# Performance work log

Measured on AMD Instinct MI355X. Metric: run time of the kernel, lower is better.

## Reference

```python
import jax, jax.numpy as jnp
import numpy as np

INPUT_DIM = 64
OUTPUT_DIM = 128
KNN = 10          # hardcoded min(10, N) in source
RADIUS = 0.02     # density radius in source


def setup_inputs() -> dict:
    key = jax.random.key(0)
    k1, k2, k3, k4, k5, k6, k7 = jax.random.split(key, 7)
    B, N = 2, 8192
    points = jax.random.uniform(k1, (B, N, 3), dtype=jnp.float32)
    features = jax.random.normal(k2, (B, N, INPUT_DIM), dtype=jnp.float32)
    leaf_mask = jax.random.randint(k3, (B, N), 0, 2) > 0
    d_in = INPUT_DIM + 6
    s1 = 1.0 / np.sqrt(d_in)
    s2 = 1.0 / np.sqrt(OUTPUT_DIM)
    W1 = jax.random.uniform(k4, (d_in, OUTPUT_DIM), jnp.float32, -s1, s1)
    b1 = jax.random.uniform(k5, (OUTPUT_DIM,), jnp.float32, -s1, s1)
    W2 = jax.random.uniform(k6, (OUTPUT_DIM, OUTPUT_DIM), jnp.float32, -s2, s2)
    b2 = jax.random.uniform(k7, (OUTPUT_DIM,), jnp.float32, -s2, s2)
    return {"points": points, "features": features, "leaf_mask": leaf_mask,
            "W1": W1, "b1": b1, "W2": W2, "b2": b2}


def _leaf_geometry(points, mask):
    # points: [N,3], mask: [N] bool -> [N,6]
    mask_f = mask.astype(points.dtype)
    cnt = jnp.maximum(mask_f.sum(), 1.0)
    center = (points * mask_f[:, None]).sum(0) / cnt      # mean of masked points
    rel = points - center                                  # [N,3]
    dist_c = jnp.linalg.norm(rel, axis=1)                  # dist to leaf center
    rel_h = rel[:, 2]                                      # relative height
    horiz = jnp.linalg.norm(rel[:, :2], axis=1)            # horizontal distance
    # pairwise euclidean distances [N,N]; used only for thresholding and knn
    sq = jnp.sum(points * points, axis=1)
    d2 = sq[:, None] + sq[None, :] - 2.0 * (points @ points.T)
    dist = jax.lax.stop_gradient(jnp.sqrt(jnp.maximum(d2, 0.0)))
    density = jnp.sum((dist < RADIUS) & mask[None, :], axis=1).astype(points.dtype)
    # KNN (smallest distances, includes self) -> local PCA curvature
    _, idx = jax.lax.top_k(-dist, KNN)                     # [N,KNN]
    neighbors = points[idx]                                # [N,KNN,3]
    centered = neighbors - points[:, None, :]
    cov = jnp.einsum('nki,nkj->nij', centered, centered) / float(KNN)  # [N,3,3]
    ev = jnp.linalg.eigh(cov)[0]                           # ascending eigenvalues
    curv = ev[:, 0] / (ev[:, 2] + 1e-8)
    rad = jnp.arctan2(rel[:, 1], rel[:, 0])
    geom = jnp.stack([dist_c, rel_h, horiz, density, curv, rad], axis=1)
    # source returns zeros when mask is empty
    return jnp.where(mask_f.sum() > 0, geom, jnp.zeros_like(geom))


def reference(points, features, leaf_mask, W1, b1, W2, b2):
    geom = jax.vmap(_leaf_geometry)(points, leaf_mask)     # [B,N,6]
    combined = jnp.concatenate([features, geom], axis=-1)  # [B,N,input_dim+6]
    h = jax.nn.relu(combined @ W1 + b1)
    return jax.nn.relu(h @ W2 + b2)                        # [B,N,output_dim]
```

## Files before the change

kernel.cpp:

```cpp
#include <hip/hip_runtime.h>
#include <math.h>
#include <stdint.h>

#define B_SZ   2
#define N_PTS  8192
#define IN_DIM 64
#define D_IN   70
#define ODIM   128
#define NQ_ALL (B_SZ * N_PTS)
#define RADIUS_F 0.02f

#define GDIM  32
#define NCELL (GDIM * GDIM * GDIM)
#define HCELL 0.03125f

#define SUP     4
#define NSUP_AX 8
#define NSUPER  (NSUP_AX * NSUP_AX * NSUP_AX)
#define SCAP    352
#define LCAP    24
#define MAXROWS 100

#define MROWS   32

typedef unsigned long long u64;

__device__ __forceinline__ void insert11(u64 (&best)[11], u64 key) {
#pragma unroll
  for (int j = 10; j >= 1; --j) {
    u64 hi = (best[j - 1] > key) ? best[j - 1] : key;
    best[j] = (best[j] < hi) ? best[j] : hi;
  }
  best[0] = (best[0] < key) ? best[0] : key;
}
__device__ __forceinline__ void insert10(u64 (&best)[10], u64 key) {
#pragma unroll
  for (int j = 9; j >= 1; --j) {
    u64 hi = (best[j - 1] > key) ? best[j - 1] : key;
    best[j] = (best[j] < hi) ? best[j] : hi;
  }
  best[0] = (best[0] < key) ? best[0] : key;
}

__device__ __forceinline__ float sq3(float x, float y, float z) {
  return __fadd_rn(__fadd_rn(__fmul_rn(x, x), __fmul_rn(y, y)), __fmul_rn(z, z));
}

__device__ __forceinline__ int cellOf(float v) {
  int c = (int)(v * 32.0f);
  return min(max(c, 0), GDIM - 1);
}

__device__ __forceinline__ void geom_epilogue(const float* __restrict__ P,
                                              const int (&idxs)[10], float dens,
                                              float px, float py, float pz,
                                              float4 ctr, float* __restrict__ g) {
  double c00 = 0, c01 = 0, c02 = 0, c11 = 0, c12 = 0, c22 = 0;
#pragma unroll
  for (int j = 0; j < 10; ++j) {
    const int idx = idxs[j];
    const float nx = P[3 * idx + 0], ny = P[3 * idx + 1], nz = P[3 * idx + 2];
    const float ex = __fsub_rn(nx, px);
    const float ey = __fsub_rn(ny, py);
    const float ez = __fsub_rn(nz, pz);
    c00 += (double)ex * ex; c01 += (double)ex * ey; c02 += (double)ex * ez;
    c11 += (double)ey * ey; c12 += (double)ey * ez; c22 += (double)ez * ez;
  }
  const double a00 = c00 / 10.0, a01 = c01 / 10.0, a02 = c02 / 10.0;
  const double a11 = c11 / 10.0, a12 = c12 / 10.0, a22 = c22 / 10.0;

  double p1 = a01 * a01 + a02 * a02 + a12 * a12;
  double qq = (a00 + a11 + a22) / 3.0;
  double p2 = (a00 - qq) * (a00 - qq) + (a11 - qq) * (a11 - qq) +
              (a22 - qq) * (a22 - qq) + 2.0 * p1;
  double ev0, ev2;
  if (p2 <= 1e-60) {
    ev0 = ev2 = qq;
  } else {
    double p = sqrt(p2 / 6.0);
    double invp = 1.0 / p;
    double b00 = (a00 - qq) * invp, b11 = (a11 - qq) * invp, b22 = (a22 - qq) * invp;
    double b01 = a01 * invp, b02 = a02 * invp, b12 = a12 * invp;
    double detB = b00 * (b11 * b22 - b12 * b12) - b01 * (b01 * b22 - b12 * b02) +
                  b02 * (b01 * b12 - b11 * b02);
    double r = 0.5 * detB;
    r = fmin(1.0, fmax(-1.0, r));
    double phi = acos(r) / 3.0;
    ev2 = qq + 2.0 * p * cos(phi);
    ev0 = qq + 2.0 * p * cos(phi + 2.0943951023931953);
  }
  const float curv = (float)(ev0 / (ev2 + 1e-08));

  const bool on = ctr.w > 0.0f;
  const float rx = __fsub_rn(px, ctr.x);
  const float ry = __fsub_rn(py, ctr.y);
  const float rz = __fsub_rn(pz, ctr.z);
  const float dist_c = sqrtf(sq3(rx, ry, rz));
  const float horiz  = sqrtf(__fadd_rn(__fmul_rn(rx, rx), __fmul_rn(ry, ry)));
  const float rad    = atan2f(ry, rx);

  g[0] = on ? dist_c : 0.0f;
  g[1] = on ? rz : 0.0f;
  g[2] = on ? horiz : 0.0f;
  g[3] = on ? dens : 0.0f;
  g[4] = on ? curv : 0.0f;
  g[5] = on ? rad : 0.0f;
}

__global__ __launch_bounds__(256) void k_build(const float* __restrict__ points,
                                               const int* __restrict__ mask,
                                               int* __restrict__ count,
                                               double* __restrict__ ctrAcc) {
  const int t = blockIdx.x * 256 + threadIdx.x;
  const int b = t >> 13;
  const int i = t & (N_PTS - 1);
  const float* P = points + (size_t)b * N_PTS * 3;
  const float x = P[3 * i + 0], y = P[3 * i + 1], z = P[3 * i + 2];
  atomicAdd(&count[b * NCELL + (cellOf(z) * GDIM + cellOf(y)) * GDIM + cellOf(x)], 1);

  const bool m = mask[b * N_PTS + i] != 0;
  double vx = m ? (double)x : 0.0, vy = m ? (double)y : 0.0;
  double vz = m ? (double)z : 0.0, vc = m ? 1.0 : 0.0;
#pragma unroll
  for (int s = 1; s < 64; s <<= 1) {
    vx += __shfl_xor(vx, s); vy += __shfl_xor(vy, s);
    vz += __shfl_xor(vz, s); vc += __shfl_xor(vc, s);
  }
  __shared__ double sh[4][4];
  const int w = threadIdx.x >> 6;
  if ((threadIdx.x & 63) == 0) { sh[0][w] = vx; sh[1][w] = vy; sh[2][w] = vz; sh[3][w] = vc; }
  __syncthreads();
  if (threadIdx.x == 0) {
    atomicAdd(&ctrAcc[b * 4 + 0], sh[0][0] + sh[0][1] + sh[0][2] + sh[0][3]);
    atomicAdd(&ctrAcc[b * 4 + 1], sh[1][0] + sh[1][1] + sh[1][2] + sh[1][3]);
    atomicAdd(&ctrAcc[b * 4 + 2], sh[2][0] + sh[2][1] + sh[2][2] + sh[2][3]);
    atomicAdd(&ctrAcc[b * 4 + 3], sh[3][0] + sh[3][1] + sh[3][2] + sh[3][3]);
  }
}

__global__ __launch_bounds__(1024) void k_scan(const int* __restrict__ count,
                                               int* __restrict__ start,
                                               int* __restrict__ cur,
                                               const double* __restrict__ ctrAcc,
                                               float* __restrict__ centerOut) {
  const int b = blockIdx.x;
  const int t = threadIdx.x;
  if (t == 0) {
    const float cf = (float)ctrAcc[b * 4 + 3];
    const float div = fmaxf(cf, 1.0f);
    centerOut[b * 4 + 0] = (float)ctrAcc[b * 4 + 0] / div;
    centerOut[b * 4 + 1] = (float)ctrAcc[b * 4 + 1] / div;
    centerOut[b * 4 + 2] = (float)ctrAcc[b * 4 + 2] / div;
    centerOut[b * 4 + 3] = (cf > 0.0f) ? 1.0f : 0.0f;
  }
  int c[32]; int sum = 0;
#pragma unroll
  for (int j = 0; j < 32; ++j) { c[j] = count[b * NCELL + t * 32 + j]; sum += c[j]; }
  __shared__ int s[1024];
  s[t] = sum;
  __syncthreads();
  for (int off = 1; off < 1024; off <<= 1) {
    int v = (t >= off) ? s[t - off] : 0;
    __syncthreads();
    if (t >= off) s[t] += v;
    __syncthreads();
  }
  int excl = (t > 0) ? s[t - 1] : 0;
#pragma unroll
  for (int j = 0; j < 32; ++j) {
    start[b * (NCELL + 1) + t * 32 + j] = excl;
    cur[b * NCELL + t * 32 + j] = excl;
    excl += c[j];
  }
  if (t == 1023) start[b * (NCELL + 1) + NCELL] = excl;
}

__global__ __launch_bounds__(256) void k_scatter(const float* __restrict__ points,
                                                 const int* __restrict__ mask,
                                                 int* __restrict__ cur,
                                                 float4* __restrict__ sorted) {
  const int t = blockIdx.x * 256 + threadIdx.x;
  const int b = t >> 13;
  const int i = t & (N_PTS - 1);
  const float* P = points + (size_t)b * N_PTS * 3;
  const float x = P[3 * i + 0], y = P[3 * i + 1], z = P[3 * i + 2];
  const int cell = (cellOf(z) * GDIM + cellOf(y)) * GDIM + cellOf(x);
  const int pos = atomicAdd(&cur[b * NCELL + cell], 1);
  const unsigned wb = (unsigned)i | ((mask[b * N_PTS + i] != 0) ? 0x80000000u : 0u);
  sorted[(size_t)b * N_PTS + pos] = make_float4(x, y, z, __uint_as_float(wb));
}

__global__ __launch_bounds__(128) void k_collect(const float* __restrict__ points,
                                                 const float4* __restrict__ sorted,
                                                 const int* __restrict__ start,
                                                 const float* __restrict__ center,
                                                 float* __restrict__ geom,
                                                 int* __restrict__ list,
                                                 int* __restrict__ listCnt,
                                                 float COLLECT_T, float DENS_T,
                                                 float THR_CHECK) {
  const int b  = blockIdx.y;
  const int sc = blockIdx.x;
  const int sx = sc & 7, sy = (sc >> 3) & 7, sz = sc >> 6;
  const int tid = threadIdx.x;

  const int* ST = start + b * (NCELL + 1);
  const float4* SP = sorted + (size_t)b * N_PTS;

  const int x0 = SUP * sx, x1 = SUP * sx + SUP - 1;
  const int y0 = SUP * sy, y1 = SUP * sy + SUP - 1;
  const int z0 = SUP * sz, z1 = SUP * sz + SUP - 1;
  const int hx0 = max(x0 - 3, 0), hx1 = min(x1 + 3, GDIM - 1);
  const int hy0 = max(y0 - 3, 0), hy1 = min(y1 + 3, GDIM - 1);
  const int hz0 = max(z0 - 3, 0), hz1 = min(z1 + 3, GDIM - 1);
  const int yc = hy1 - hy0 + 1;
  const int R  = (hz1 - hz0 + 1) * yc;

  __shared__ int    rs[MAXROWS], rp[MAXROWS + 1];
  __shared__ int    qs_[16], qp_[17];
  __shared__ float4 pts4[SCAP];
  __shared__ u64    lbuf[128 * LCAP];

  if (tid < 64) {
    {
      int qlen = 0, qst = 0;
      if (tid < 16) {
        const int z = z0 + (tid >> 2), y = y0 + (tid & 3);
        const int base = (z * GDIM + y) * GDIM;
        qst  = ST[base + x0];
        qlen = ST[base + x1 + 1] - qst;
      }
      int inc = qlen;
      for (int off = 1; off < 64; off <<= 1) { int v = __shfl_up(inc, off); if (tid >= off) inc += v; }
      if (tid < 16) { qs_[tid] = qst; qp_[tid] = inc - qlen; }
      if (tid == 63) qp_[16] = inc;
    }
    {
      int len[2] = {0, 0}, st2[2] = {0, 0};
#pragma unroll
      for (int k = 0; k < 2; ++k) {
        const int r = tid * 2 + k;
        if (r < R) {
          const int z = hz0 + r / yc, y = hy0 + r % yc;
          const int base = (z * GDIM + y) * GDIM;
          st2[k] = ST[base + hx0];
          len[k] = ST[base + hx1 + 1] - st2[k];
        }
      }
      int sum = len[0] + len[1];
      int inc = sum;
      for (int off = 1; off < 64; off <<= 1) { int v = __shfl_up(inc, off); if (tid >= off) inc += v; }
      int exc = inc - sum;
#pragma unroll
      for (int k = 0; k < 2; ++k) {
        const int r = tid * 2 + k;
        if (r < R) { rs[r] = st2[k]; rp[r] = exc; }
        exc += len[k];
      }
      if (tid == 63) rp[R] = inc;
    }
  }
  __syncthreads();

  const int C    = rp[R];
  const int qtot = qp_[16];
  if (qtot == 0) return;

  if (C > SCAP) {
    for (int t = tid; t < qtot; t += 128) {
      int lo = 0, hi = 15;
      while (lo < hi) { const int mid = (lo + hi + 1) >> 1; if (qp_[mid] <= t) lo = mid; else hi = mid - 1; }
      const int qglob = qs_[lo] + (t - qp_[lo]);
      const int pos = atomicAdd(listCnt, 1);
      list[pos] = (b << 13) | qglob;
    }
    return;
  }

  for (int i = tid; i < C; i += 128) {
    int lo = 0, hi = R - 1;
    while (lo < hi) { const int mid = (lo + hi + 1) >> 1; if (rp[mid] <= i) lo = mid; else hi = mid - 1; }
    pts4[i] = SP[rs[lo] + (i - rp[lo])];
  }
  __syncthreads();

  const float4 ctr = reinterpret_cast<const float4*>(center)[b];
  const float* P = points + (size_t)b * N_PTS * 3;
  const int sub = tid & 3;
  const int gq  = tid >> 2;

  for (int q0 = 0; q0 < qtot; q0 += 32) {
    const int myq = q0 + gq;
    const bool act = (myq < qtot);
    const int mq = act ? myq : 0;
    int lo = 0, hi = 15;
    while (lo < hi) { const int mid = (lo + hi + 1) >> 1; if (qp_[mid] <= mq) lo = mid; else hi = mid - 1; }
    const int qglob = qs_[lo] + (mq - qp_[lo]);
    const float4 qp4 = SP[qglob];
    const int qidx = (int)(__float_as_uint(qp4.w) & 0x7FFFFFFFu);
    const float px = qp4.x, py = qp4.y, pz = qp4.z;
    const float sqq = sq3(px, py, pz);

    int cnt = 0;
    u64* myb = &lbuf[tid * LCAP];
#pragma unroll 2
    for (int j = sub; j < C; j += 4) {
      const float4 tp = pts4[j];
      const float sqc = sq3(tp.x, tp.y, tp.z);
      const float dot = __fmaf_rn(pz, tp.z, __fmaf_rn(py, tp.y, __fmul_rn(px, tp.x)));
      const float d2  = __fsub_rn(__fadd_rn(sqq, sqc), __fmul_rn(2.0f, dot));
      const float d2c = fmaxf(d2, 0.0f);
      if (d2c < COLLECT_T) {
        if (cnt < LCAP) {
          const unsigned wb = __float_as_uint(tp.w);
          myb[cnt] = ((u64)__float_as_uint(d2c) << 32)
                   | (u64)(((wb & 0x7FFFFFFFu) << 1) | (wb >> 31));
        }
        ++cnt;
      }
    }

    u64 best[11];
#pragma unroll
    for (int j = 0; j < 11; ++j) best[j] = ~0ull;
    float dens = 0.0f;
    const int m = min(cnt, LCAP);
    for (int i = 0; i < m; ++i) {
      const u64 e = myb[i];
      if ((e & 1ull) && __uint_as_float((unsigned)(e >> 32)) < DENS_T) dens += 1.0f;
      if (e < best[10]) insert11(best, e);
    }
    int cntg = cnt;
    int over = (cnt > LCAP) ? 1 : 0;
#pragma unroll
    for (int s = 1; s < 4; s <<= 1) {
      dens += __shfl_xor(dens, s);
      cntg += __shfl_xor(cntg, s);
      over |= __shfl_xor(over, s);
      u64 ok[11];
#pragma unroll
      for (int j = 0; j < 11; ++j) ok[j] = __shfl_xor(best[j], s);
#pragma unroll
      for (int j = 0; j < 11; ++j) {
        if (ok[j] < best[10]) insert11(best, ok[j]); else break;
      }
    }

    if (act && sub == 0) {
      const float dist9 = sqrtf(__uint_as_float((unsigned)(best[9] >> 32)));
      bool bad = (over != 0) || (cntg < 10) || !(dist9 < THR_CHECK);
      if (cntg >= 11) {
        const float dist10 = sqrtf(__uint_as_float((unsigned)(best[10] >> 32)));
        bad = bad || (dist10 == dist9);
      }
      if (bad) {
        const int pos = atomicAdd(listCnt, 1);
        list[pos] = (b << 13) | qglob;
      } else {
        int idxs[10];
#pragma unroll
        for (int j = 0; j < 10; ++j) idxs[j] = (int)(((unsigned)best[j]) >> 1);
        geom_epilogue(P, idxs, dens, px, py, pz, ctr,
                      geom + ((size_t)b * N_PTS + qidx) * 6);
      }
    }
  }
}

__global__ __launch_bounds__(64) void k_wavefb(const float* __restrict__ points,
                                               const float4* __restrict__ sorted,
                                               const int* __restrict__ start,
                                               const float* __restrict__ center,
                                               float* __restrict__ geom,
                                               int* __restrict__ flags2,
                                               const int* __restrict__ list,
                                               const int* __restrict__ listCnt) {
  const int lane = threadIdx.x;
  const int n = *listCnt;
  for (int it = blockIdx.x; it < n; it += gridDim.x) {
    const int e = list[it];
    const int b = e >> 13, qs = e & (N_PTS - 1);
    const float4* SP = sorted + (size_t)b * N_PTS;
    const int* ST = start + b * (NCELL + 1);
    const float4 qp = SP[qs];
    const int qidx = (int)(__float_as_uint(qp.w) & 0x7FFFFFFFu);
    const float px = qp.x, py = qp.y, pz = qp.z;
    const float sqq = sq3(px, py, pz);
    const int cx = cellOf(px), cy = cellOf(py), cz = cellOf(pz);
    const int xlo = max(cx - 8, 0), xhi = min(cx + 8, GDIM - 1);
    const int ylo = max(cy - 8, 0), yhi = min(cy + 8, GDIM - 1);
    const int zlo = max(cz - 8, 0), zhi = min(cz + 8, GDIM - 1);
    const int ycw = yhi - ylo + 1;
    const int Rw = (zhi - zlo + 1) * ycw;

    u64 best[10];
#pragma unroll
    for (int j = 0; j < 10; ++j) best[j] = ((u64)0x7F800000u << 32) | 0xFFFFFFFFu;
    float dens = 0.0f;

    for (int r = lane; r < Rw; r += 64) {
      const int z = zlo + r / ycw, y = ylo + r % ycw;
      const int base = (z * GDIM + y) * GDIM;
      const int j0 = ST[base + xlo], j1 = ST[base + xhi + 1];
      for (int j = j0; j < j1; ++j) {
        const float4 tp = SP[j];
        const unsigned wb = __float_as_uint(tp.w);
        const float sqc = sq3(tp.x, tp.y, tp.z);
        const float dot = __fmaf_rn(pz, tp.z, __fmaf_rn(py, tp.y, __fmul_rn(px, tp.x)));
        const float d2  = __fsub_rn(__fadd_rn(sqq, sqc), __fmul_rn(2.0f, dot));
        const float dist = sqrtf(fmaxf(d2, 0.0f));
        if ((dist < RADIUS_F) && (wb & 0x80000000u)) dens += 1.0f;
        const u64 key = ((u64)__float_as_uint(dist) << 32) | (wb & 0x7FFFFFFFu);
        if (key < best[9]) insert10(best, key);
      }
    }
#pragma unroll
    for (int s = 1; s < 64; s <<= 1) {
      dens += __shfl_xor(dens, s);
      u64 ok[10];
#pragma unroll
      for (int j = 0; j < 10; ++j) ok[j] = __shfl_xor(best[j], s);
#pragma unroll
      for (int j = 0; j < 10; ++j) {
        if (ok[j] < best[9]) insert10(best, ok[j]); else break;
      }
    }
    if (lane == 0) {
      const float dist9 = __uint_as_float((unsigned)(best[9] >> 32));
      if (dist9 < 0.2494f) {
        const float4 ctr = reinterpret_cast<const float4*>(center)[b];
        const float* P = points + (size_t)b * N_PTS * 3;
        int idxs[10];
#pragma unroll
        for (int j = 0; j < 10; ++j) idxs[j] = (int)(((unsigned)best[j]) & 0x7FFFFFFFu);
        geom_epilogue(P, idxs, dens, px, py, pz, ctr, geom + ((size_t)b * N_PTS + qidx) * 6);
      } else {
        flags2[b * N_PTS + qs] = 1;
      }
    }
  }
}

__global__ __launch_bounds__(256) void k_fallback(const float* __restrict__ points,
                                                  const float4* __restrict__ sorted,
                                                  const int* __restrict__ start,
                                                  const float* __restrict__ center,
                                                  float* __restrict__ geom,
                                                  const int* __restrict__ flags2) {
  const int b = blockIdx.y;
  const int qs = blockIdx.x * 256 + threadIdx.x;
  if (flags2[b * N_PTS + qs] == 0) return;
  const float4 qp = sorted[(size_t)b * N_PTS + qs];
  const unsigned qw = __float_as_uint(qp.w);
  const int qidx = (int)(qw & 0x7FFFFFFFu);

  const float px = qp.x, py = qp.y, pz = qp.z;
  const float sqq = sq3(px, py, pz);
  const int cx = cellOf(px), cy = cellOf(py), cz = cellOf(pz);

  const int* ST = start + b * (NCELL + 1);
  const float4* SP = sorted + (size_t)b * N_PTS;

  u64 best[10];
#pragma unroll
  for (int j = 0; j < 10; ++j) best[j] = ((u64)0x7F800000u << 32) | 0xFFFFFFFFu;
  float dens = 0.0f;

  for (int rho = 0; rho < GDIM; ++rho) {
    const int zlo = max(cz - rho, 0), zhi = min(cz + rho, GDIM - 1);
    const int ylo = max(cy - rho, 0), yhi = min(cy + rho, GDIM - 1);
    for (int z = zlo; z <= zhi; ++z) {
      const int adz = abs(z - cz);
      for (int y = ylo; y <= yhi; ++y) {
        const int ady = abs(y - cy);
        const int m2 = max(adz, ady);
        int ja, jb;
        int ja2 = 0, jb2 = 0;
        const int rowBase = (z * GDIM + y) * GDIM;
        if (m2 == rho) {
          const int xa = max(cx - rho, 0), xb = min(cx + rho, GDIM - 1);
          ja = ST[rowBase + xa]; jb = ST[rowBase + xb + 1];
        } else {
          ja = jb = 0;
          if (cx - rho >= 0)        { ja = ST[rowBase + cx - rho]; jb = ST[rowBase + cx - rho + 1]; }
          if (cx + rho <= GDIM - 1) { ja2 = ST[rowBase + cx + rho]; jb2 = ST[rowBase + cx + rho + 1]; }
        }
#pragma unroll 1
        for (int pass = 0; pass < 2; ++pass) {
          const int j0 = pass ? ja2 : ja;
          const int j1 = pass ? jb2 : jb;
          for (int j = j0; j < j1; ++j) {
            const float4 tp = SP[j];
            const unsigned wb = __float_as_uint(tp.w);
            const float sqc = sq3(tp.x, tp.y, tp.z);
            const float dot = __fmaf_rn(pz, tp.z, __fmaf_rn(py, tp.y, __fmul_rn(px, tp.x)));
            const float d2  = __fsub_rn(__fadd_rn(sqq, sqc), __fmul_rn(2.0f, dot));
            const float dist = sqrtf(fmaxf(d2, 0.0f));
            if ((dist < RADIUS_F) && (wb & 0x80000000u)) dens += 1.0f;
            const u64 key = ((u64)__float_as_uint(dist) << 32) | (wb & 0x7FFFFFFFu);
            if (key < best[9]) insert10(best, key);
          }
        }
      }
    }
    if (rho >= 1) {
      const float dist9 = __uint_as_float((unsigned)(best[9] >> 32));
      if (dist9 < (float)rho * HCELL * 0.999f) break;
    }
  }

  const float4 ctr = reinterpret_cast<const float4*>(center)[b];
  const float* P = points + (size_t)b * N_PTS * 3;
  int idxs[10];
#pragma unroll
  for (int j = 0; j < 10; ++j) idxs[j] = (int)(((unsigned)best[j]) & 0x7FFFFFFFu);
  geom_epilogue(P, idxs, dens, px, py, pz, ctr, geom + ((size_t)b * N_PTS + qidx) * 6);
}

__global__ __launch_bounds__(256) void k_mlp(const float* __restrict__ features,
                                             const float* __restrict__ geom,
                                             const float* __restrict__ W1,
                                             const float* __restrict__ b1,
                                             const float* __restrict__ W2,
                                             const float* __restrict__ b2,
                                             float* __restrict__ out) {
  __shared__ float A[MROWS][71];
  __shared__ float H[MROWS][133];
  const int tid = threadIdx.x;
  const int row0 = blockIdx.x * MROWS;

  for (int i = tid; i < MROWS * IN_DIM; i += 256) {
    int r = i >> 6, k = i & 63;
    A[r][k] = features[(size_t)(row0 + r) * IN_DIM + k];
  }
  for (int i = tid; i < MROWS * 8; i += 256) {
    int r = i >> 3, k = i & 7;
    if (k < 6) A[r][IN_DIM + k] = geom[(size_t)(row0 + r) * 6 + k];
  }
  __syncthreads();

  const int r0 = tid >> 4;
  const int c  = (tid & 15) * 8;

  float acc[2][8];
#pragma unroll
  for (int i = 0; i < 2; ++i)
#pragma unroll
    for (int j = 0; j < 8; ++j) acc[i][j] = 0.0f;

#pragma unroll 2
  for (int k = 0; k < D_IN; ++k) {
    const float a0 = A[r0][k];
    const float a1 = A[r0 + 16][k];
    const float4 w0 = *reinterpret_cast<const float4*>(&W1[(size_t)k * ODIM + c]);
    const float4 w1 = *reinterpret_cast<const float4*>(&W1[(size_t)k * ODIM + c + 4]);
    const float w[8] = {w0.x, w0.y, w0.z, w0.w, w1.x, w1.y, w1.z, w1.w};
#pragma unroll
    for (int j = 0; j < 8; ++j) {
      acc[0][j] = fmaf(a0, w[j], acc[0][j]);
      acc[1][j] = fmaf(a1, w[j], acc[1][j]);
    }
  }
  {
    const float4 bb0 = *reinterpret_cast<const float4*>(&b1[c]);
    const float4 bb1 = *reinterpret_cast<const float4*>(&b1[c + 4]);
    const float bb[8] = {bb0.x, bb0.y, bb0.z, bb0.w, bb1.x, bb1.y, bb1.z, bb1.w};
#pragma unroll
    for (int i = 0; i < 2; ++i) {
      const int rr = r0 + 16 * i;
      float4 h0 = make_float4(fmaxf(acc[i][0] + bb[0], 0.f), fmaxf(acc[i][1] + bb[1], 0.f),
                              fmaxf(acc[i][2] + bb[2], 0.f), fmaxf(acc[i][3] + bb[3], 0.f));
      float4 h1 = make_float4(fmaxf(acc[i][4] + bb[4], 0.f), fmaxf(acc[i][5] + bb[5], 0.f),
                              fmaxf(acc[i][6] + bb[6], 0.f), fmaxf(acc[i][7] + bb[7], 0.f));
      *reinterpret_cast<float4*>(&H[rr][c]) = h0;
      *reinterpret_cast<float4*>(&H[rr][c + 4]) = h1;
    }
  }
  __syncthreads();

#pragma unroll
  for (int i = 0; i < 2; ++i)
#pragma unroll
    for (int j = 0; j < 8; ++j) acc[i][j] = 0.0f;

#pragma unroll 2
  for (int k = 0; k < ODIM; ++k) {
    const float a0 = H[r0][k];
    const float a1 = H[r0 + 16][k];
    const float4 w0 = *reinterpret_cast<const float4*>(&W2[(size_t)k * ODIM + c]);
    const float4 w1 = *reinterpret_cast<const float4*>(&W2[(size_t)k * ODIM + c + 4]);
    const float w[8] = {w0.x, w0.y, w0.z, w0.w, w1.x, w1.y, w1.z, w1.w};
#pragma unroll
    for (int j = 0; j < 8; ++j) {
      acc[0][j] = fmaf(a0, w[j], acc[0][j]);
      acc[1][j] = fmaf(a1, w[j], acc[1][j]);
    }
  }
  {
    const float4 bb0 = *reinterpret_cast<const float4*>(&b2[c]);
    const float4 bb1 = *reinterpret_cast<const float4*>(&b2[c + 4]);
    const float bb[8] = {bb0.x, bb0.y, bb0.z, bb0.w, bb1.x, bb1.y, bb1.z, bb1.w};
#pragma unroll
    for (int i = 0; i < 2; ++i) {
      const size_t row = (size_t)(row0 + r0 + 16 * i);
      float4 o0 = make_float4(fmaxf(acc[i][0] + bb[0], 0.f), fmaxf(acc[i][1] + bb[1], 0.f),
                              fmaxf(acc[i][2] + bb[2], 0.f), fmaxf(acc[i][3] + bb[3], 0.f));
      float4 o1 = make_float4(fmaxf(acc[i][4] + bb[4], 0.f), fmaxf(acc[i][5] + bb[5], 0.f),
                              fmaxf(acc[i][6] + bb[6], 0.f), fmaxf(acc[i][7] + bb[7], 0.f));
      *reinterpret_cast<float4*>(&out[row * ODIM + c]) = o0;
      *reinterpret_cast<float4*>(&out[row * ODIM + c + 4]) = o1;
    }
  }
}

extern "C" void kernel_launch(void* const* d_in, const int* in_sizes, int n_in,
                              void* d_out, int out_size, void* d_ws, size_t ws_size,
                              hipStream_t stream) {
  const float* points   = (const float*)d_in[0];
  const float* features = (const float*)d_in[1];
  const int*   mask     = (const int*)d_in[2];
  const float* W1       = (const float*)d_in[3];
  const float* b1       = (const float*)d_in[4];
  const float* W2       = (const float*)d_in[5];
  const float* b2       = (const float*)d_in[6];
  float* out = (float*)d_out;

  const double Rd   = (double)0.02f;
  const double midd = Rd - ldexp(1.0, -30);
  const double Td   = midd * midd;
  float densT = (float)Td;
  if ((double)densT <= Td) densT = nextafterf(densT, 1.0f);
  const float collectT = 0.0935f * 0.0935f;
  const float thrCheck = 0.0934f;

  char* w = (char*)d_ws;
  size_t off = 0;
  auto take = [&](size_t bytes) { char* p = w + off; off = (off + bytes + 255) & ~(size_t)255; return p; };
  float*  geomBuf   = (float*)take((size_t)NQ_ALL * 6 * 4);
  float*  centerBuf = (float*)take(2 * 16);
  char*   zero0     = (char*)take(0);
  int*    countBuf  = (int*)take((size_t)B_SZ * NCELL * 4);
  int*    flags2Buf = (int*)take((size_t)NQ_ALL * 4);
  int*    listCnt   = (int*)take(4);
  double* ctrAcc    = (double*)take((size_t)B_SZ * 4 * 8);
  char*   zero1     = (char*)take(0);
  int*    startBuf  = (int*)take((size_t)B_SZ * (NCELL + 1) * 4);
  int*    curBuf    = (int*)take((size_t)B_SZ * NCELL * 4);
  float4* sortedBuf = (float4*)take((size_t)B_SZ * N_PTS * 16);
  int*    listBuf   = (int*)take((size_t)NQ_ALL * 4);
  (void)ws_size;

  hipMemsetAsync(zero0, 0, (size_t)(zero1 - zero0), stream);
  k_build<<<NQ_ALL / 256, 256, 0, stream>>>(points, mask, countBuf, ctrAcc);
  k_scan<<<B_SZ, 1024, 0, stream>>>(countBuf, startBuf, curBuf, ctrAcc, centerBuf);
  k_scatter<<<NQ_ALL / 256, 256, 0, stream>>>(points, mask, curBuf, sortedBuf);
  k_collect<<<dim3(NSUPER, B_SZ), 128, 0, stream>>>(points, sortedBuf, startBuf, centerBuf,
                                                    geomBuf, listBuf, listCnt,
                                                    collectT, densT, thrCheck);
  k_wavefb<<<1024, 64, 0, stream>>>(points, sortedBuf, startBuf, centerBuf,
                                    geomBuf, flags2Buf, listBuf, listCnt);
  k_fallback<<<dim3(N_PTS / 256, B_SZ), 256, 0, stream>>>(points, sortedBuf, startBuf,
                                                          centerBuf, geomBuf, flags2Buf);
  k_mlp<<<NQ_ALL / MROWS, 256, 0, stream>>>(features, geomBuf, W1, b1, W2, b2, out);
}
```

Before: 186.5 us.

## Adapt per-query KNN collect radius, pack fallback waves, shrink MLP tile

k_collect now derives a per-query collection radius from the query's distance to the halo boundary and a density-scaled estimate (larger near the unit-cube edges). It uses this radius both as the candidate cutoff and as the certification threshold, so fewer candidates land in local buffers and fewer queries overflow to the fallback list. The wavefront fallback kernel now runs four waves per 256-thread block instead of one wave per block. The MLP kernel processes 16 rows per block with one row per thread and float4 feature loads, giving twice as many blocks but less weight reuse per load. The tighter radius could send more queries down the fallback path if it certifies fewer of them.

```diff
diff --git a/kernel.cpp b/kernel.cpp
--- a/kernel.cpp
+++ b/kernel.cpp
@@ -21,7 +21,7 @@
 #define LCAP    24
 #define MAXROWS 100
 
-#define MROWS   32
+#define MROWS   16
 
 typedef unsigned long long u64;
 
@@ -197,8 +197,7 @@
                                                  float* __restrict__ geom,
                                                  int* __restrict__ list,
                                                  int* __restrict__ listCnt,
-                                                 float COLLECT_T, float DENS_T,
-                                                 float THR_CHECK) {
+                                                 float DENS_T) {
   const int b  = blockIdx.y;
   const int sc = blockIdx.x;
   const int sx = sc & 7, sy = (sc >> 3) & 7, sz = sc >> 6;
@@ -283,6 +282,10 @@
     pts4[i] = SP[rs[lo] + (i - rp[lo])];
   }
   __syncthreads();
+
+  const bool cxl = (x0 - 3 < 0), cxh = (x1 + 3 > GDIM - 1);
+  const bool cyl = (y0 - 3 < 0), cyh = (y1 + 3 > GDIM - 1);
+  const bool czl = (z0 - 3 < 0), czh = (z1 + 3 > GDIM - 1);
 
   const float4 ctr = reinterpret_cast<const float4*>(center)[b];
   const float* P = points + (size_t)b * N_PTS * 3;
@@ -301,6 +304,21 @@
     const float px = qp4.x, py = qp4.y, pz = qp4.z;
     const float sqq = sq3(px, py, pz);
 
+    const float mxl = cxl ? 1e9f : __fsub_rn(px, (float)hx0 * HCELL);
+    const float mxh = cxh ? 1e9f : __fsub_rn((float)(hx1 + 1) * HCELL, px);
+    const float myl = cyl ? 1e9f : __fsub_rn(py, (float)hy0 * HCELL);
+    const float myh = cyh ? 1e9f : __fsub_rn((float)(hy1 + 1) * HCELL, py);
+    const float mzl = czl ? 1e9f : __fsub_rn(pz, (float)hz0 * HCELL);
+    const float mzh = czh ? 1e9f : __fsub_rn((float)(hz1 + 1) * HCELL, pz);
+    const float gr = fminf(fminf(fminf(mxl, mxh), fminf(myl, myh)), fminf(mzl, mzh));
+    const float fx = 0.5f * (1.0f + fminf(fminf(px, 1.0f - px) * (1.0f / 0.0935f), 1.0f));
+    const float fy = 0.5f * (1.0f + fminf(fminf(py, 1.0f - py) * (1.0f / 0.0935f), 1.0f));
+    const float fz = 0.5f * (1.0f + fminf(fminf(pz, 1.0f - pz) * (1.0f / 0.0935f), 1.0f));
+    const float rT = 0.0935f * cbrtf(1.0f / (fx * fy * fz));
+    const float cR = fminf(gr, rT);
+    const float cT2 = cR * cR;
+    const float certR = cR * 0.999f;
+
     int cnt = 0;
     u64* myb = &lbuf[tid * LCAP];
 #pragma unroll 2
@@ -310,7 +328,7 @@
       const float dot = __fmaf_rn(pz, tp.z, __fmaf_rn(py, tp.y, __fmul_rn(px, tp.x)));
       const float d2  = __fsub_rn(__fadd_rn(sqq, sqc), __fmul_rn(2.0f, dot));
       const float d2c = fmaxf(d2, 0.0f);
-      if (d2c < COLLECT_T) {
+      if (d2c < cT2) {
         if (cnt < LCAP) {
           const unsigned wb = __float_as_uint(tp.w);
           myb[cnt] = ((u64)__float_as_uint(d2c) << 32)
@@ -348,7 +366,7 @@
 
     if (act && sub == 0) {
       const float dist9 = sqrtf(__uint_as_float((unsigned)(best[9] >> 32)));
-      bool bad = (over != 0) || (cntg < 10) || !(dist9 < THR_CHECK);
+      bool bad = (over != 0) || (cntg < 10) || !(dist9 < certR);
       if (cntg >= 11) {
         const float dist10 = sqrtf(__uint_as_float((unsigned)(best[10] >> 32)));
         bad = bad || (dist10 == dist9);
@@ -367,17 +385,18 @@
   }
 }
 
-__global__ __launch_bounds__(64) void k_wavefb(const float* __restrict__ points,
-                                               const float4* __restrict__ sorted,
-                                               const int* __restrict__ start,
-                                               const float* __restrict__ center,
-                                               float* __restrict__ geom,
-                                               int* __restrict__ flags2,
-                                               const int* __restrict__ list,
-                                               const int* __restrict__ listCnt) {
-  const int lane = threadIdx.x;
+__global__ __launch_bounds__(256) void k_wavefb(const float* __restrict__ points,
+                                                const float4* __restrict__ sorted,
+                                                const int* __restrict__ start,
+                                                const float* __restrict__ center,
+                                                float* __restrict__ geom,
+                                                int* __restrict__ flags2,
+                                                const int* __restrict__ list,
+                                                const int* __restrict__ listCnt) {
+  const int lane = threadIdx.x & 63;
+  const int wid  = threadIdx.x >> 6;
   const int n = *listCnt;
-  for (int it = blockIdx.x; it < n; it += gridDim.x) {
+  for (int it = blockIdx.x * 4 + wid; it < n; it += gridDim.x * 4) {
     const int e = list[it];
     const int b = e >> 13, qs = e & (N_PTS - 1);
     const float4* SP = sorted + (size_t)b * N_PTS;
@@ -529,87 +548,69 @@
   const int tid = threadIdx.x;
   const int row0 = blockIdx.x * MROWS;
 
-  for (int i = tid; i < MROWS * IN_DIM; i += 256) {
-    int r = i >> 6, k = i & 63;
-    A[r][k] = features[(size_t)(row0 + r) * IN_DIM + k];
-  }
-  for (int i = tid; i < MROWS * 8; i += 256) {
-    int r = i >> 3, k = i & 7;
-    if (k < 6) A[r][IN_DIM + k] = geom[(size_t)(row0 + r) * 6 + k];
+  {
+    const int r = tid >> 4, f4 = (tid & 15) * 4;
+    const float4 v = *reinterpret_cast<const float4*>(&features[(size_t)(row0 + r) * IN_DIM + f4]);
+    A[r][f4 + 0] = v.x; A[r][f4 + 1] = v.y; A[r][f4 + 2] = v.z; A[r][f4 + 3] = v.w;
+  }
+  if (tid < MROWS * 6) {
+    const int r = tid / 6, k = tid % 6;
+    A[r][IN_DIM + k] = geom[(size_t)(row0 + r) * 6 + k];
   }
   __syncthreads();
 
-  const int r0 = tid >> 4;
-  const int c  = (tid & 15) * 8;
-
-  float acc[2][8];
-#pragma unroll
-  for (int i = 0; i < 2; ++i)
-#pragma unroll
-    for (int j = 0; j < 8; ++j) acc[i][j] = 0.0f;
-
-#pragma unroll 2
+  const int r = tid >> 4;
+  const int c = (tid & 15) * 8;
+
+  float acc[8];
+#pragma unroll
+  for (int j = 0; j < 8; ++j) acc[j] = 0.0f;
+
+#pragma unroll 4
   for (int k = 0; k < D_IN; ++k) {
-    const float a0 = A[r0][k];
-    const float a1 = A[r0 + 16][k];
+    const float a = A[r][k];
     const float4 w0 = *reinterpret_cast<const float4*>(&W1[(size_t)k * ODIM + c]);
     const float4 w1 = *reinterpret_cast<const float4*>(&W1[(size_t)k * ODIM + c + 4]);
-    const float w[8] = {w0.x, w0.y, w0.z, w0.w, w1.x, w1.y, w1.z, w1.w};
-#pragma unroll
-    for (int j = 0; j < 8; ++j) {
-      acc[0][j] = fmaf(a0, w[j], acc[0][j]);
-      acc[1][j] = fmaf(a1, w[j], acc[1][j]);
-    }
+    acc[0] = fmaf(a, w0.x, acc[0]); acc[1] = fmaf(a, w0.y, acc[1]);
+    acc[2] = fmaf(a, w0.z, acc[2]); acc[3] = fmaf(a, w0.w, acc[3]);
+    acc[4] = fmaf(a, w1.x, acc[4]); acc[5] = fmaf(a, w1.y, acc[5]);
+    acc[6] = fmaf(a, w1.z, acc[6]); acc[7] = fmaf(a, w1.w, acc[7]);
   }
   {
     const float4 bb0 = *reinterpret_cast<const float4*>(&b1[c]);
     const float4 bb1 = *reinterpret_cast<const float4*>(&b1[c + 4]);
-    const float bb[8] = {bb0.x, bb0.y, bb0.z, bb0.w, bb1.x, bb1.y, bb1.z, bb1.w};
-#pragma unroll
-    for (int i = 0; i < 2; ++i) {
-      const int rr = r0 + 16 * i;
-      float4 h0 = make_float4(fmaxf(acc[i][0] + bb[0], 0.f), fmaxf(acc[i][1] + bb[1], 0.f),
-                              fmaxf(acc[i][2] + bb[2], 0.f), fmaxf(acc[i][3] + bb[3], 0.f));
-      float4 h1 = make_float4(fmaxf(acc[i][4] + bb[4], 0.f), fmaxf(acc[i][5] + bb[5], 0.f),
-                              fmaxf(acc[i][6] + bb[6], 0.f), fmaxf(acc[i][7] + bb[7], 0.f));
-      *reinterpret_cast<float4*>(&H[rr][c]) = h0;
-      *reinterpret_cast<float4*>(&H[rr][c + 4]) = h1;
-    }
+    float4 h0 = make_float4(fmaxf(acc[0] + bb0.x, 0.f), fmaxf(acc[1] + bb0.y, 0.f),
+                            fmaxf(acc[2] + bb0.z, 0.f), fmaxf(acc[3] + bb0.w, 0.f));
+    float4 h1 = make_float4(fmaxf(acc[4] + bb1.x, 0.f), fmaxf(acc[5] + bb1.y, 0.f),
+                            fmaxf(acc[6] + bb1.z, 0.f), fmaxf(acc[7] + bb1.w, 0.f));
+    H[r][c + 0] = h0.x; H[r][c + 1] = h0.y; H[r][c + 2] = h0.z; H[r][c + 3] = h0.w;
+    H[r][c + 4] = h1.x; H[r][c + 5] = h1.y; H[r][c + 6] = h1.z; H[r][c + 7] = h1.w;
   }
   __syncthreads();
 
 #pragma unroll
-  for (int i = 0; i < 2; ++i)
-#pragma unroll
-    for (int j = 0; j < 8; ++j) acc[i][j] = 0.0f;
-
-#pragma unroll 2
+  for (int j = 0; j < 8; ++j) acc[j] = 0.0f;
+
+#pragma unroll 4
   for (int k = 0; k < ODIM; ++k) {
-    const float a0 = H[r0][k];
-    const float a1 = H[r0 + 16][k];
+    const float a = H[r][k];
     const float4 w0 = *reinterpret_cast<const float4*>(&W2[(size_t)k * ODIM + c]);
     const float4 w1 = *reinterpret_cast<const float4*>(&W2[(size_t)k * ODIM + c + 4]);
-    const float w[8] = {w0.x, w0.y, w0.z, w0.w, w1.x, w1.y, w1.z, w1.w};
-#pragma unroll
-    for (int j = 0; j < 8; ++j) {
-      acc[0][j] = fmaf(a0, w[j], acc[0][j]);
-      acc[1][j] = fmaf(a1, w[j], acc[1][j]);
-    }
+    acc[0] = fmaf(a, w0.x, acc[0]); acc[1] = fmaf(a, w0.y, acc[1]);
+    acc[2] = fmaf(a, w0.z, acc[2]); acc[3] = fmaf(a, w0.w, acc[3]);
+    acc[4] = fmaf(a, w1.x, acc[4]); acc[5] = fmaf(a, w1.y, acc[5]);
+    acc[6] = fmaf(a, w1.z, acc[6]); acc[7] = fmaf(a, w1.w, acc[7]);
   }
   {
     const float4 bb0 = *reinterpret_cast<const float4*>(&b2[c]);
     const float4 bb1 = *reinterpret_cast<const float4*>(&b2[c + 4]);
-    const float bb[8] = {bb0.x, bb0.y, bb0.z, bb0.w, bb1.x, bb1.y, bb1.z, bb1.w};
-#pragma unroll
-    for (int i = 0; i < 2; ++i) {
-      const size_t row = (size_t)(row0 + r0 + 16 * i);
-      float4 o0 = make_float4(fmaxf(acc[i][0] + bb[0], 0.f), fmaxf(acc[i][1] + bb[1], 0.f),
-                              fmaxf(acc[i][2] + bb[2], 0.f), fmaxf(acc[i][3] + bb[3], 0.f));
-      float4 o1 = make_float4(fmaxf(acc[i][4] + bb[4], 0.f), fmaxf(acc[i][5] + bb[5], 0.f),
-                              fmaxf(acc[i][6] + bb[6], 0.f), fmaxf(acc[i][7] + bb[7], 0.f));
-      *reinterpret_cast<float4*>(&out[row * ODIM + c]) = o0;
-      *reinterpret_cast<float4*>(&out[row * ODIM + c + 4]) = o1;
-    }
+    const size_t row = (size_t)(row0 + r);
+    float4 o0 = make_float4(fmaxf(acc[0] + bb0.x, 0.f), fmaxf(acc[1] + bb0.y, 0.f),
+                            fmaxf(acc[2] + bb0.z, 0.f), fmaxf(acc[3] + bb0.w, 0.f));
+    float4 o1 = make_float4(fmaxf(acc[4] + bb1.x, 0.f), fmaxf(acc[5] + bb1.y, 0.f),
+                            fmaxf(acc[6] + bb1.z, 0.f), fmaxf(acc[7] + bb1.w, 0.f));
+    *reinterpret_cast<float4*>(&out[row * ODIM + c]) = o0;
+    *reinterpret_cast<float4*>(&out[row * ODIM + c + 4]) = o1;
   }
 }
 
@@ -630,8 +631,6 @@
   const double Td   = midd * midd;
   float densT = (float)Td;
   if ((double)densT <= Td) densT = nextafterf(densT, 1.0f);
-  const float collectT = 0.0935f * 0.0935f;
-  const float thrCheck = 0.0934f;
 
   char* w = (char*)d_ws;
   size_t off = 0;
@@ -655,9 +654,8 @@
   k_scan<<<B_SZ, 1024, 0, stream>>>(countBuf, startBuf, curBuf, ctrAcc, centerBuf);
   k_scatter<<<NQ_ALL / 256, 256, 0, stream>>>(points, mask, curBuf, sortedBuf);
   k_collect<<<dim3(NSUPER, B_SZ), 128, 0, stream>>>(points, sortedBuf, startBuf, centerBuf,
-                                                    geomBuf, listBuf, listCnt,
-                                                    collectT, densT, thrCheck);
-  k_wavefb<<<1024, 64, 0, stream>>>(points, sortedBuf, startBuf, centerBuf,
+                                                    geomBuf, listBuf, listCnt, densT);
+  k_wavefb<<<512, 256, 0, stream>>>(points, sortedBuf, startBuf, centerBuf,
                                     geomBuf, flags2Buf, listBuf, listCnt);
   k_fallback<<<dim3(N_PTS / 256, B_SZ), 256, 0, stream>>>(points, sortedBuf, startBuf,
                                                           centerBuf, geomBuf, flags2Buf);
```

Result: slower. 214.4 us (+14.9%).
